# Kernel optimization log

Measured on AMD Instinct MI355X. Metric: run time of the kernel, lower is better.

The kernel has to match this reference:

```python
import jax, jax.numpy as jnp
import numpy as np

N = 20000       # num_nodes
B = 4           # batch
D = 32          # input_dim
OUT = 64        # output_dim
S = 2           # n_supports
E = 640000      # edges per support (avg degree 32)
MAX_STEP = 3
M = MAX_STEP * S + 1  # num_metrics = 7


def setup_inputs() -> dict:
    key = jax.random.key(0)
    k = jax.random.split(key, 6)
    inputs = jax.random.normal(k[0], (B, N, D), dtype=jnp.float32)
    edge_src = jax.random.randint(k[1], (S, E), 0, N, dtype=jnp.int32)
    edge_dst = jax.random.randint(k[2], (S, E), 0, N, dtype=jnp.int32)
    # ~1/deg scaled values so the diffusion recurrence stays numerically tame
    edge_vals = jax.random.uniform(k[3], (S, E), dtype=jnp.float32) / 32.0
    W = jax.random.normal(k[4], (OUT, D * M), dtype=jnp.float32) * 0.05
    bias = jnp.zeros((OUT,), dtype=jnp.float32)
    return dict(inputs=inputs, edge_vals=edge_vals, W=W, bias=bias,
                edge_src=edge_src, edge_dst=edge_dst)


def _spmm(vals, src, dst, x):
    # y[i] = sum_{edges (i<-j)} vals * x[j]  == support.mm(x) for COO support
    return jax.ops.segment_sum(vals[:, None] * x[src], dst, num_segments=N)


def reference(inputs, edge_vals, W, bias, edge_src, edge_dst):
    b, n, d = inputs.shape
    # x0: [N, D*B], batch fastest (matches permute([1,2,0]).reshape(n,-1))
    x0 = jnp.transpose(inputs, (1, 2, 0)).reshape(n, -1)
    xs = [x0]
    for s in range(S):
        v, sr, ds = edge_vals[s], edge_src[s], edge_dst[s]
        x1 = _spmm(v, sr, ds, x0)
        xs.append(x1)
        for _ in range(2, MAX_STEP + 1):
            x2 = 2.0 * _spmm(v, sr, ds, x1) - x0
            xs.append(x2)
            # NOTE: faithful to source aliasing quirk — x0 is mutated here,
            # so the next support starts from the mutated x0.
            x1, x0 = x2, x1
    x = jnp.stack(xs, 0)                       # [M, N, D*B]
    x = x.reshape(-1, n, d, b)                 # [M, N, D, B]
    x = jnp.transpose(x, (3, 1, 2, 0))         # [B, N, D, M]
    x = x.reshape(b, n, -1)                    # [B, N, D*M], M fastest
    return x @ W.T + bias                      # [B, N, OUT]
```

## Files before the change

### kernel.cpp

```cpp
#include <hip/hip_runtime.h>

#define N_NODES 20000
#define BATCH   4
#define DIN     32
#define DOUT    64
#define MSTEPS  7
#define ROW     128
#define NROW    896
#define NROWU   448
#define PLN     656
#define NT      79
#define KB2     (2 * NT)
#define CHUNK   2048
#define SLOT    12288
#define WSLOT   3584
#define RGRID   (N_NODES / 4)
#define PGRID   625
#define TGRID   1250

typedef short  short8 __attribute__((ext_vector_type(8)));
typedef float  f32x4  __attribute__((ext_vector_type(4)));

__device__ __forceinline__ unsigned short f2bf(float f) {
    unsigned u = __float_as_uint(f);
    unsigned r = u + 0x7fff + ((u >> 16) & 1);
    return (unsigned short)(r >> 16);
}
__device__ __forceinline__ float bf_lo(unsigned p) { return __uint_as_float(p << 16); }
__device__ __forceinline__ float bf_hi(unsigned p) { return __uint_as_float(p & 0xffff0000u); }

__global__ void init_k(int* __restrict__ cursor) {
    if (threadIdx.x < KB2) cursor[threadIdx.x] = threadIdx.x * SLOT;
}

__global__ void __launch_bounds__(256) p2t_k(const int* __restrict__ src,
                                             const int* __restrict__ dst,
                                             const float* __restrict__ vals,
                                             int* __restrict__ cursor,
                                             uint2* __restrict__ staged,
                                             const float* __restrict__ in,
                                             unsigned short* __restrict__ xs, int E) {
    __shared__ int lhist[KB2];
    __shared__ int lbase[KB2];
    __shared__ int gbase[KB2];
    __shared__ int sc[256];
    __shared__ uint2 buf[CHUNK];
    __shared__ unsigned short kk[CHUNK];
    int t = threadIdx.x;
    if (blockIdx.x >= PGRID) {
        int tid = (blockIdx.x - PGRID) * 256 + t;
        if (tid < N_NODES * 16) {
            int dq = tid & 3;
            int b  = (tid >> 2) & 3;
            int n  = tid >> 4;
            int d0 = dq * 8;
            const float* ip = in + ((size_t)b * N_NODES + n) * DIN + d0;
            float4 f0 = *(const float4*)ip;
            float4 f1 = *(const float4*)(ip + 4);
            uint4 o;
            o.x = (unsigned)f2bf(f0.x) | ((unsigned)f2bf(f0.y) << 16);
            o.y = (unsigned)f2bf(f0.z) | ((unsigned)f2bf(f0.w) << 16);
            o.z = (unsigned)f2bf(f1.x) | ((unsigned)f2bf(f1.y) << 16);
            o.w = (unsigned)f2bf(f1.z) | ((unsigned)f2bf(f1.w) << 16);
            *(uint4*)(xs + (size_t)n * NROW + b * 32 + d0) = o;
        }
        return;
    }
    int base = blockIdx.x * CHUNK;
    int nval = min(CHUNK, 2 * E - base);
    for (int i = t; i < KB2; i += 256) lhist[i] = 0;
    __syncthreads();
    int k[CHUNK / 256], pos[CHUNK / 256];
    uint2 pay[CHUNK / 256];
#pragma unroll
    for (int j = 0; j < CHUNK / 256; ++j) {
        int i = j * 256 + t;
        int e = base + i;
        if (i < nval) {
            int s = (e >= E) ? 1 : 0;
            int d = dst[e];
            pay[j] = make_uint2((unsigned)src[e] | ((unsigned)f2bf(vals[e]) << 16),
                                (unsigned)d);
            k[j] = s * NT + (d >> 8);
            pos[j] = atomicAdd(&lhist[k[j]], 1);
        } else k[j] = -1;
    }
    __syncthreads();
    int v = (t < KB2) ? lhist[t] : 0;
    sc[t] = v;
    __syncthreads();
    for (int off = 1; off < 256; off <<= 1) {
        int a = (t >= off) ? sc[t - off] : 0;
        __syncthreads();
        sc[t] += a;
        __syncthreads();
    }
    if (t < KB2) lbase[t] = sc[t] - v;
    __syncthreads();
    if (t < KB2 && lhist[t]) gbase[t] = atomicAdd(&cursor[t], lhist[t]);
#pragma unroll
    for (int j = 0; j < CHUNK / 256; ++j) {
        if (k[j] >= 0) {
            int slot = lbase[k[j]] + pos[j];
            buf[slot] = pay[j];
            kk[slot] = (unsigned short)k[j];
        }
    }
    __syncthreads();
#pragma unroll
    for (int j = 0; j < CHUNK / 256; ++j) {
        int i = j * 256 + t;
        if (i < nval) {
            int b = kk[i];
            staged[gbase[b] + (i - lbase[b])] = buf[i];
        }
    }
}

__global__ void __launch_bounds__(256) p3_fine_k(const uint2* __restrict__ staged,
                                                 const int* __restrict__ cursor,
                                                 int2* __restrict__ row_desc,
                                                 unsigned* __restrict__ csr) {
    __shared__ int lhist[64];
    __shared__ int sc[64];
    __shared__ int lcur[64];
    int bb = blockIdx.x;
    int b = bb >> 2, sub = bb & 3;
    int s = b / NT, tile = b - s * NT;
    int w0loc = sub * 64;
    int seg0 = b * SLOT;
    int len = cursor[b] - seg0;
    int t = threadIdx.x;
    if (t < 64) lhist[t] = 0;
    __syncthreads();
    for (int i = t; i < len; i += 256) {
        int dl = (int)(staged[seg0 + i].y & 255) - w0loc;
        if (dl >= 0 && dl < 64) atomicAdd(&lhist[dl], 1);
    }
    __syncthreads();
    int cntr = (t < 64) ? lhist[t] : 0;
    int pl = (cntr + 15) & ~15;
    if (t < 64) sc[t] = pl;
    __syncthreads();
    for (int off = 1; off < 64; off <<= 1) {
        int a = (t < 64 && t >= off) ? sc[t - off] : 0;
        __syncthreads();
        if (t < 64) sc[t] += a;
        __syncthreads();
    }
    int wbase = bb * WSLOT;
    if (t < 64) {
        int excl = sc[t] - pl;
        lcur[t] = wbase + excl;
        int nd = tile * 256 + w0loc + t;
        if (nd < N_NODES) row_desc[s * N_NODES + nd] = make_int2(wbase + excl, pl);
    }
    __syncthreads();
    for (int i = t; i < len; i += 256) {
        uint2 u = staged[seg0 + i];
        int dl = (int)(u.y & 255) - w0loc;
        if (dl >= 0 && dl < 64) {
            int p = atomicAdd(&lcur[dl], 1);
            csr[p] = u.x;
        }
    }
    if (t < 64) {
        int excl = sc[t] - pl;
        for (int i = cntr; i < pl; ++i) csr[wbase + excl + i] = 0u;
    }
}

__device__ __forceinline__ void issue16(const unsigned* __restrict__ csr, int e,
                                        const unsigned* __restrict__ xb, int lane,
                                        unsigned c[16], unsigned p[16]) {
    uint4 q0 = *(const uint4*)(csr + e);
    uint4 q1 = *(const uint4*)(csr + e + 4);
    uint4 q2 = *(const uint4*)(csr + e + 8);
    uint4 q3 = *(const uint4*)(csr + e + 12);
    c[0]=q0.x;  c[1]=q0.y;  c[2]=q0.z;  c[3]=q0.w;
    c[4]=q1.x;  c[5]=q1.y;  c[6]=q1.z;  c[7]=q1.w;
    c[8]=q2.x;  c[9]=q2.y;  c[10]=q2.z; c[11]=q2.w;
    c[12]=q3.x; c[13]=q3.y; c[14]=q3.z; c[15]=q3.w;
#pragma unroll
    for (int j = 0; j < 16; ++j)
        p[j] = xb[(size_t)(c[j] & 0xffffu) * NROWU + lane];
}

__device__ __forceinline__ void fmac16(const unsigned c[16], const unsigned p[16],
                                       float acc[8]) {
#pragma unroll
    for (int j = 0; j < 16; ++j) {
        float v = bf_hi(c[j]);
        acc[j & 3]       = fmaf(v, bf_lo(p[j]), acc[j & 3]);
        acc[4 + (j & 3)] = fmaf(v, bf_hi(p[j]), acc[4 + (j & 3)]);
    }
}

__device__ __forceinline__ void spmm_core(const int2* __restrict__ rdesc,
                                          const unsigned* __restrict__ csr,
                                          const unsigned* __restrict__ xb,
                                          const unsigned* __restrict__ xprevb,
                                          unsigned* __restrict__ yb,
                                          float alpha, int node, int lane) {
    int2 rd = rdesc[node];
    int start = rd.x, len = rd.y;
    float acc[8];
#pragma unroll
    for (int j = 0; j < 8; ++j) acc[j] = 0.f;
    if (len) {
        unsigned cA[16], pA[16], cB[16], pB[16];
        int n16 = len >> 4;
        issue16(csr, start, xb, lane, cA, pA);
        int k = 1;
        for (; k + 1 < n16; k += 2) {
            issue16(csr, start + k * 16, xb, lane, cB, pB);
            fmac16(cA, pA, acc);
            issue16(csr, start + (k + 1) * 16, xb, lane, cA, pA);
            fmac16(cB, pB, acc);
        }
        if (k < n16) {
            issue16(csr, start + k * 16, xb, lane, cB, pB);
            fmac16(cA, pA, acc);
            fmac16(cB, pB, acc);
        } else {
            fmac16(cA, pA, acc);
        }
    }
    float r0 = alpha * ((acc[0] + acc[1]) + (acc[2] + acc[3]));
    float r1 = alpha * ((acc[4] + acc[5]) + (acc[6] + acc[7]));
    if (xprevb) {
        unsigned pp = xprevb[(size_t)node * NROWU + lane];
        r0 -= bf_lo(pp);
        r1 -= bf_hi(pp);
    }
    yb[(size_t)node * NROWU + lane] = (unsigned)f2bf(r0) | ((unsigned)f2bf(r1) << 16);
}

__global__ void __launch_bounds__(256) spmm_row_k(const int2* __restrict__ rdesc,
                                                  const unsigned* __restrict__ csr,
                                                  const unsigned short* __restrict__ x,
                                                  const unsigned short* __restrict__ xprev,
                                                  unsigned short* __restrict__ y, float alpha) {
    int node = __builtin_amdgcn_readfirstlane(blockIdx.x * 4 + (threadIdx.x >> 6));
    int lane = threadIdx.x & 63;
    spmm_core(rdesc, csr, (const unsigned*)x, (const unsigned*)xprev, (unsigned*)y,
              alpha, node, lane);
}

__global__ void __launch_bounds__(256) spmm_dual_k(const int2* __restrict__ rdA,
                                                   const int2* __restrict__ rdB,
                                                   const unsigned* __restrict__ csr,
                                                   const unsigned short* __restrict__ x,
                                                   const unsigned short* __restrict__ xprevA,
                                                   unsigned short* __restrict__ yA,
                                                   unsigned short* __restrict__ yB) {
    int bid = blockIdx.x;
    int second = (bid >= RGRID) ? 1 : 0;
    int node = __builtin_amdgcn_readfirstlane((bid - second * RGRID) * 4 + (threadIdx.x >> 6));
    int lane = threadIdx.x & 63;
    const int2* rd = second ? rdB : rdA;
    const unsigned* xprevb = second ? nullptr : (const unsigned*)xprevA;
    unsigned* yb = second ? (unsigned*)yB : (unsigned*)yA;
    float alpha = second ? 1.0f : 2.0f;
    spmm_core(rd, csr, (const unsigned*)x, xprevb, yb, alpha, node, lane);
}

__global__ void __launch_bounds__(256) epilogue_mfma_k(const unsigned short* __restrict__ xs,
                                                       const float* __restrict__ W,
                                                       const float* __restrict__ bias,
                                                       float* __restrict__ out) {
    __shared__ unsigned short Alds[28 * PLN];
    int tid = threadIdx.x;
    int lane = tid & 63, ot = tid >> 6;
    int col = lane & 15, quad = lane >> 4;
    int o = ot * 16 + col;

    short8 bfrag[MSTEPS];
#pragma unroll
    for (int m = 0; m < MSTEPS; ++m) {
        short8 bf;
#pragma unroll
        for (int j = 0; j < 8; ++j)
            bf[j] = (short)f2bf(W[o * 224 + (quad * 8 + j) * 7 + m]);
        bfrag[m] = bf;
    }
    float bo = bias[o];

    int n0 = blockIdx.x * 16;
    const uint4* src = (const uint4*)(xs + (size_t)n0 * NROW);
#pragma unroll
    for (int it = 0; it < 7; ++it) {
        int idx = tid + it * 256;
        uint4 q = src[idx];
        int r   = idx / 112;
        int rem = idx - r * 112;
        int m   = rem >> 4;
        int b   = (rem >> 2) & 3;
        int d0  = (rem & 3) * 8;
        *(uint4*)&Alds[(b * 7 + m) * PLN + r * 40 + d0] = q;
    }
    __syncthreads();

    f32x4 acc[BATCH];
#pragma unroll
    for (int b = 0; b < BATCH; ++b)
        acc[b] = (f32x4){bo, bo, bo, bo};

#pragma unroll
    for (int m = 0; m < MSTEPS; ++m) {
#pragma unroll
        for (int b = 0; b < BATCH; ++b) {
            short8 a = *(const short8*)&Alds[(b * 7 + m) * PLN + col * 40 + quad * 8];
            acc[b] = __builtin_amdgcn_mfma_f32_16x16x32_bf16(a, bfrag[m], acc[b], 0, 0, 0);
        }
    }

#pragma unroll
    for (int b = 0; b < BATCH; ++b) {
#pragma unroll
        for (int reg = 0; reg < 4; ++reg) {
            int n = n0 + quad * 4 + reg;
            out[((size_t)b * N_NODES + n) * DOUT + o] = acc[b][reg];
        }
    }
}

extern "C" void kernel_launch(void* const* d_in, const int* in_sizes, int n_in,
                              void* d_out, int out_size, void* d_ws, size_t ws_size,
                              hipStream_t stream) {
    const float* inputs    = (const float*)d_in[0];
    const float* edge_vals = (const float*)d_in[1];
    const float* W         = (const float*)d_in[2];
    const float* bias      = (const float*)d_in[3];
    const int*   edge_src  = (const int*)d_in[4];
    const int*   edge_dst  = (const int*)d_in[5];
    float* out = (float*)d_out;
    const int E = in_sizes[1] / 2;

    unsigned short* xs = (unsigned short*)d_ws;
    uint2* staged  = (uint2*)(xs + (size_t)N_NODES * NROW);
    unsigned* csr  = (unsigned*)(staged + (size_t)KB2 * SLOT);
    int* cursor    = (int*)(csr + (size_t)4 * KB2 * WSLOT);
    int2* row_desc = (int2*)(cursor + KB2 + 2);

    const int epgrid = N_NODES / 16;

    init_k<<<1, 256, 0, stream>>>(cursor);
    p2t_k<<<PGRID + TGRID, 256, 0, stream>>>(edge_src, edge_dst, edge_vals, cursor,
                                             staged, inputs, xs, E);
    p3_fine_k<<<4 * KB2, 256, 0, stream>>>(staged, cursor, row_desc, csr);

    const int2* rd0 = row_desc;
    const int2* rd1 = row_desc + N_NODES;

    unsigned short* X0 = xs + 0 * ROW;
    unsigned short* X1 = xs + 1 * ROW;
    unsigned short* X2 = xs + 2 * ROW;
    unsigned short* X3 = xs + 3 * ROW;
    unsigned short* X4 = xs + 4 * ROW;
    unsigned short* X5 = xs + 5 * ROW;
    unsigned short* X6 = xs + 6 * ROW;

    spmm_row_k<<<RGRID, 256, 0, stream>>>(rd0, csr, X0, nullptr, X1, 1.0f);
    spmm_row_k<<<RGRID, 256, 0, stream>>>(rd0, csr, X1, X0,      X2, 2.0f);
    spmm_dual_k<<<2 * RGRID, 256, 0, stream>>>(rd0, rd1, csr, X2, X1, X3, X4);
    spmm_row_k<<<RGRID, 256, 0, stream>>>(rd1, csr, X4, X2, X5, 2.0f);
    spmm_row_k<<<RGRID, 256, 0, stream>>>(rd1, csr, X5, X4, X6, 2.0f);

    epilogue_mfma_k<<<epgrid, 256, 0, stream>>>(xs, W, bias, out);
}
```

Measured before the change: 227.9 us.

## Pre-convert W to bf16, load epilogue A directly, and shrink SpMM batch to 8

W is converted to bf16 once in the init kernel, in MFMA fragment order, so each epilogue block loads contiguous short8 fragments instead of doing strided fp32 gathers and conversions. The epilogue drops its LDS staging and barrier and reads A fragments straight from global memory. The SpMM inner loop now gathers 8 edges per step instead of 16, which cuts register pressure and padding waste but leaves fewer loads in flight per wave. Rows whose padded length is not a multiple of 8 could still lose edges if the CSR padding was sized for groups of 16.

```diff
diff --git a/kernel.cpp b/kernel.cpp
--- a/kernel.cpp
+++ b/kernel.cpp
@@ -8,7 +8,6 @@
 #define ROW     128
 #define NROW    896
 #define NROWU   448
-#define PLN     656
 #define NT      79
 #define KB2     (2 * NT)
 #define CHUNK   2048
@@ -29,8 +28,17 @@
 __device__ __forceinline__ float bf_lo(unsigned p) { return __uint_as_float(p << 16); }
 __device__ __forceinline__ float bf_hi(unsigned p) { return __uint_as_float(p & 0xffff0000u); }
 
-__global__ void init_k(int* __restrict__ cursor) {
-    if (threadIdx.x < KB2) cursor[threadIdx.x] = threadIdx.x * SLOT;
+__global__ void init_k(int* __restrict__ cursor, const float* __restrict__ W,
+                       unsigned short* __restrict__ Wbf) {
+    if (blockIdx.x == 0) {
+        if (threadIdx.x < KB2) cursor[threadIdx.x] = threadIdx.x * SLOT;
+        return;
+    }
+    int i = (int)(blockIdx.x - 1) * 256 + threadIdx.x;
+    int m = i >> 11;
+    int o = (i >> 5) & 63;
+    int c = i & 31;
+    Wbf[i] = f2bf(W[o * 224 + c * 7 + m]);
 }
 
 __global__ void __launch_bounds__(256) p2t_k(const int* __restrict__ src,
@@ -170,26 +178,22 @@
     }
 }
 
-__device__ __forceinline__ void issue16(const unsigned* __restrict__ csr, int e,
-                                        const unsigned* __restrict__ xb, int lane,
-                                        unsigned c[16], unsigned p[16]) {
+__device__ __forceinline__ void issue8(const unsigned* __restrict__ csr, int e,
+                                       const unsigned* __restrict__ xb, int lane,
+                                       unsigned c[8], unsigned p[8]) {
     uint4 q0 = *(const uint4*)(csr + e);
     uint4 q1 = *(const uint4*)(csr + e + 4);
-    uint4 q2 = *(const uint4*)(csr + e + 8);
-    uint4 q3 = *(const uint4*)(csr + e + 12);
-    c[0]=q0.x;  c[1]=q0.y;  c[2]=q0.z;  c[3]=q0.w;
-    c[4]=q1.x;  c[5]=q1.y;  c[6]=q1.z;  c[7]=q1.w;
-    c[8]=q2.x;  c[9]=q2.y;  c[10]=q2.z; c[11]=q2.w;
-    c[12]=q3.x; c[13]=q3.y; c[14]=q3.z; c[15]=q3.w;
-#pragma unroll
-    for (int j = 0; j < 16; ++j)
+    c[0]=q0.x; c[1]=q0.y; c[2]=q0.z; c[3]=q0.w;
+    c[4]=q1.x; c[5]=q1.y; c[6]=q1.z; c[7]=q1.w;
+#pragma unroll
+    for (int j = 0; j < 8; ++j)
         p[j] = xb[(size_t)(c[j] & 0xffffu) * NROWU + lane];
 }
 
-__device__ __forceinline__ void fmac16(const unsigned c[16], const unsigned p[16],
-                                       float acc[8]) {
-#pragma unroll
-    for (int j = 0; j < 16; ++j) {
+__device__ __forceinline__ void fmac8(const unsigned c[8], const unsigned p[8],
+                                      float acc[8]) {
+#pragma unroll
+    for (int j = 0; j < 8; ++j) {
         float v = bf_hi(c[j]);
         acc[j & 3]       = fmaf(v, bf_lo(p[j]), acc[j & 3]);
         acc[4 + (j & 3)] = fmaf(v, bf_hi(p[j]), acc[4 + (j & 3)]);
@@ -208,22 +212,22 @@
 #pragma unroll
     for (int j = 0; j < 8; ++j) acc[j] = 0.f;
     if (len) {
-        unsigned cA[16], pA[16], cB[16], pB[16];
-        int n16 = len >> 4;
-        issue16(csr, start, xb, lane, cA, pA);
+        unsigned cA[8], pA[8], cB[8], pB[8];
+        int n8 = len >> 3;
+        issue8(csr, start, xb, lane, cA, pA);
         int k = 1;
-        for (; k + 1 < n16; k += 2) {
-            issue16(csr, start + k * 16, xb, lane, cB, pB);
-            fmac16(cA, pA, acc);
-            issue16(csr, start + (k + 1) * 16, xb, lane, cA, pA);
-            fmac16(cB, pB, acc);
-        }
-        if (k < n16) {
-            issue16(csr, start + k * 16, xb, lane, cB, pB);
-            fmac16(cA, pA, acc);
-            fmac16(cB, pB, acc);
+        for (; k + 1 < n8; k += 2) {
+            issue8(csr, start + k * 8, xb, lane, cB, pB);
+            fmac8(cA, pA, acc);
+            issue8(csr, start + (k + 1) * 8, xb, lane, cA, pA);
+            fmac8(cB, pB, acc);
+        }
+        if (k < n8) {
+            issue8(csr, start + k * 8, xb, lane, cB, pB);
+            fmac8(cA, pA, acc);
+            fmac8(cB, pB, acc);
         } else {
-            fmac16(cA, pA, acc);
+            fmac8(cA, pA, acc);
         }
     }
     float r0 = alpha * ((acc[0] + acc[1]) + (acc[2] + acc[3]));
@@ -266,10 +270,9 @@
 }
 
 __global__ void __launch_bounds__(256) epilogue_mfma_k(const unsigned short* __restrict__ xs,
-                                                       const float* __restrict__ W,
+                                                       const unsigned short* __restrict__ Wbf,
                                                        const float* __restrict__ bias,
                                                        float* __restrict__ out) {
-    __shared__ unsigned short Alds[28 * PLN];
     int tid = threadIdx.x;
     int lane = tid & 63, ot = tid >> 6;
     int col = lane & 15, quad = lane >> 4;
@@ -277,29 +280,12 @@
 
     short8 bfrag[MSTEPS];
 #pragma unroll
-    for (int m = 0; m < MSTEPS; ++m) {
-        short8 bf;
-#pragma unroll
-        for (int j = 0; j < 8; ++j)
-            bf[j] = (short)f2bf(W[o * 224 + (quad * 8 + j) * 7 + m]);
-        bfrag[m] = bf;
-    }
+    for (int m = 0; m < MSTEPS; ++m)
+        bfrag[m] = *(const short8*)&Wbf[m * 2048 + o * 32 + quad * 8];
     float bo = bias[o];
 
     int n0 = blockIdx.x * 16;
-    const uint4* src = (const uint4*)(xs + (size_t)n0 * NROW);
-#pragma unroll
-    for (int it = 0; it < 7; ++it) {
-        int idx = tid + it * 256;
-        uint4 q = src[idx];
-        int r   = idx / 112;
-        int rem = idx - r * 112;
-        int m   = rem >> 4;
-        int b   = (rem >> 2) & 3;
-        int d0  = (rem & 3) * 8;
-        *(uint4*)&Alds[(b * 7 + m) * PLN + r * 40 + d0] = q;
-    }
-    __syncthreads();
+    const unsigned short* arow = xs + (size_t)(n0 + col) * NROW + quad * 8;
 
     f32x4 acc[BATCH];
 #pragma unroll
@@ -310,7 +296,7 @@
     for (int m = 0; m < MSTEPS; ++m) {
 #pragma unroll
         for (int b = 0; b < BATCH; ++b) {
-            short8 a = *(const short8*)&Alds[(b * 7 + m) * PLN + col * 40 + quad * 8];
+            short8 a = *(const short8*)&arow[m * 128 + b * 32];
             acc[b] = __builtin_amdgcn_mfma_f32_16x16x32_bf16(a, bfrag[m], acc[b], 0, 0, 0);
         }
     }
@@ -342,10 +328,11 @@
     unsigned* csr  = (unsigned*)(staged + (size_t)KB2 * SLOT);
     int* cursor    = (int*)(csr + (size_t)4 * KB2 * WSLOT);
     int2* row_desc = (int2*)(cursor + KB2 + 2);
+    unsigned short* Wbf = (unsigned short*)(row_desc + 2 * N_NODES);
 
     const int epgrid = N_NODES / 16;
 
-    init_k<<<1, 256, 0, stream>>>(cursor);
+    init_k<<<57, 256, 0, stream>>>(cursor, W, Wbf);
     p2t_k<<<PGRID + TGRID, 256, 0, stream>>>(edge_src, edge_dst, edge_vals, cursor,
                                              staged, inputs, xs, E);
     p3_fine_k<<<4 * KB2, 256, 0, stream>>>(staged, cursor, row_desc, csr);
@@ -367,5 +354,5 @@
     spmm_row_k<<<RGRID, 256, 0, stream>>>(rd1, csr, X4, X2, X5, 2.0f);
     spmm_row_k<<<RGRID, 256, 0, stream>>>(rd1, csr, X5, X4, X6, 2.0f);
 
-    epilogue_mfma_k<<<epgrid, 256, 0, stream>>>(xs, W, bias, out);
-}
+    epilogue_mfma_k<<<epgrid, 256, 0, stream>>>(xs, Wbf, bias, out);
+}
```

Measured after the change: 238.5 us. +4.6%, slower.
